# Performance work log

Hardware: AMD Instinct MI355X
Metric: run time of the kernel (lower is better)

## Reference

```python
import jax, jax.numpy as jnp
import numpy as np

ATOL = 1e-06
RTOL = 1e-06

def setup_inputs() -> dict:
    key = jax.random.key(0)
    ks = jax.random.split(key, 8)
    u = lambda k, shape: jax.random.uniform(k, shape, jnp.float32, -0.05, 0.05)
    return {
        "x": jax.random.normal(ks[0], (4096, 32, 32, 3), jnp.float32),
        "W_lstm": u(ks[1], (3, 16)),      # input kernel, gates [i,f,c,o]
        "U_lstm": u(ks[2], (4, 16)),      # recurrent kernel
        "dw_kernel": u(ks[3], (27, 27, 3, 5)),  # depthwise (kh,kw,in_c,mult)
        "pw_kernel": u(ks[4], (15, 4)),   # pointwise
        "conv_bias": u(ks[5], (4,)),
        "W_td": u(ks[6], (4096, 10)),
        "W_sc": u(ks[7], (4096, 10)),
    }

def _lstm_td(x, W, U):
    # TimeDistributed LSTM: x (B,32,32,3) -> treat axis1 as TD batch, axis2 as time
    B = x.shape[0]
    seq = x.reshape(B * 32, 32, 3)          # (N, T, F)
    xs = jnp.transpose(seq, (1, 0, 2))      # (T, N, F)
    N = seq.shape[0]
    h0 = jnp.zeros((N, 4), x.dtype)
    c0 = jnp.zeros((N, 4), x.dtype)

    def step(carry, xt):
        h, c = carry
        z = xt @ W + h @ U                  # (N, 16)
        zi, zf, zc, zo = jnp.split(z, 4, axis=-1)
        i = jax.nn.elu(zi)                  # recurrent_activation='elu'
        f = jax.nn.elu(zf)
        c = f * c + i * jax.nn.softmax(zc, axis=-1)  # activation='softmax'
        o = jax.nn.elu(zo)
        h = o * jax.nn.softmax(c, axis=-1)
        return (h, c), h

    _, hs = jax.lax.scan(step, (h0, c0), xs)        # (T, N, 4)
    return jnp.transpose(hs, (1, 0, 2)).reshape(B, 32, 32, 4)

def _sep_conv(x, dw_kernel, pw_kernel, conv_bias):
    # depthwise: Keras (kh,kw,C,M) -> lax HWIO grouped (kh,kw,1,C*M), channel-major order
    dw = dw_kernel.reshape(27, 27, 1, 15)
    y = jax.lax.conv_general_dilated(
        x, dw, window_strides=(1, 1), padding='SAME',
        feature_group_count=3,
        dimension_numbers=('NHWC', 'HWIO', 'NHWC'))   # (B,32,32,15)
    y = jnp.einsum('bhwc,cf->bhwf', y, pw_kernel) + conv_bias
    return jax.nn.sigmoid(y)                          # (B,32,32,4)

def reference(x, W_lstm, U_lstm, dw_kernel, pw_kernel, conv_bias, W_td, W_sc):
    B = x.shape[0]
    td = _lstm_td(x, W_lstm, U_lstm).reshape(B, -1) @ W_td   # (B,10)
    sc = _sep_conv(x, dw_kernel, pw_kernel, conv_bias).reshape(B, -1) @ W_sc
    diff = jnp.abs(td - sc)
    tol = ATOL + RTOL * jnp.abs(sc)
    return diff <= tol
```

## Files before the change

### kernel.cpp

```cpp
#include <hip/hip_runtime.h>
#include <math.h>

#define TD_OFF 0
#define WTDR_OFF 40960
#define BG_BYTE_OFF 524288

typedef __bf16 bf16x8 __attribute__((ext_vector_type(8)));
typedef float f32x16 __attribute__((ext_vector_type(16)));

union FragU { bf16x8 v; float4 f; };

__device__ __forceinline__ f32x16 mfma16(bf16x8 a, bf16x8 b, f32x16 c) {
    return __builtin_amdgcn_mfma_f32_32x32x16_bf16(a, b, c, 0, 0, 0);
}

__device__ __forceinline__ float eluf(float v) {
    return v > 0.f ? v : __expf(v) - 1.f;
}

__global__ __launch_bounds__(256) void prep(const float* __restrict__ dw,
                                            const float* __restrict__ pw,
                                            const float* __restrict__ Wtd,
                                            float* __restrict__ Wtdr,
                                            unsigned short* __restrict__ Bg) {
    int gid = blockIdx.x * 256 + threadIdx.x;
    if (gid < 40960) {
        int k = gid & 3;
        int r = gid >> 2;
        int row = r & 31; r >>= 5;
        int j = r % 10;
        int tt = r / 10;
        Wtdr[gid] = Wtd[(size_t)(row * 128 + tt * 4 + k) * 10 + j];
        return;
    }
    int g2 = gid - 40960;
    if (g2 >= 162 * 128) return;
    int n = g2 & 127;
    int s = g2 >> 7;
    int half = s & 1;
    int cd = s >> 1;
    int c = cd / 27, d = cd % 27;
    int w = n >> 2, f = n & 3;
    unsigned short* dsth = Bg + (size_t)s * 4096 + n * 16;
    unsigned short* dstl = dsth + 2048;
#pragma unroll
    for (int k = 0; k < 16; k++) {
        int xi = half * 16 + k;
        int dx = xi - w + 13;
        float v = 0.f;
        if (dx >= 0 && dx < 27) {
#pragma unroll
            for (int m = 0; m < 5; m++)
                v = fmaf(dw[((d * 27 + dx) * 3 + c) * 5 + m],
                         pw[(c * 5 + m) * 4 + f], v);
        }
        __bf16 h = (__bf16)v;
        __bf16 l = (__bf16)(v - (float)h);
        dsth[k] = __builtin_bit_cast(unsigned short, h);
        dstl[k] = __builtin_bit_cast(unsigned short, l);
    }
}

__global__ void lstm_td(const float* __restrict__ x,
                        const float* __restrict__ W,
                        const float* __restrict__ U,
                        const float* __restrict__ Wtdr,
                        float* __restrict__ td_out) {
    float rW[48], rU[64];
    const float4* W4 = (const float4*)W;
    const float4* U4 = (const float4*)U;
#pragma unroll
    for (int i = 0; i < 12; i++) {
        float4 q = W4[i];
        rW[i * 4 + 0] = q.x; rW[i * 4 + 1] = q.y;
        rW[i * 4 + 2] = q.z; rW[i * 4 + 3] = q.w;
    }
#pragma unroll
    for (int i = 0; i < 16; i++) {
        float4 q = U4[i];
        rU[i * 4 + 0] = q.x; rU[i * 4 + 1] = q.y;
        rU[i * 4 + 2] = q.z; rU[i * 4 + 3] = q.w;
    }

    int t = threadIdx.x;
    int n = blockIdx.x * 256 + t;
    int row = n & 31;
    const float4* xp4 = (const float4*)(x + (size_t)n * 96);

    float h0 = 0, h1 = 0, h2 = 0, h3 = 0;
    float c0 = 0, c1 = 0, c2 = 0, c3 = 0;
    float acc[10];
#pragma unroll
    for (int j = 0; j < 10; j++) acc[j] = 0.f;

    for (int g = 0; g < 8; g++) {
        float4 q0 = xp4[g * 3 + 0], q1 = xp4[g * 3 + 1], q2 = xp4[g * 3 + 2];
        float xr[12] = {q0.x, q0.y, q0.z, q0.w, q1.x, q1.y,
                        q1.z, q1.w, q2.x, q2.y, q2.z, q2.w};
#pragma unroll
        for (int st = 0; st < 4; st++) {
            int tt = g * 4 + st;
            float x0 = xr[st * 3 + 0], x1 = xr[st * 3 + 1], x2 = xr[st * 3 + 2];
            float z[16];
#pragma unroll
            for (int k = 0; k < 16; k++)
                z[k] = x0 * rW[k] + x1 * rW[16 + k] + x2 * rW[32 + k]
                     + h0 * rU[k] + h1 * rU[16 + k] + h2 * rU[32 + k] + h3 * rU[48 + k];

            float ig0 = eluf(z[0]),  ig1 = eluf(z[1]),  ig2 = eluf(z[2]),  ig3 = eluf(z[3]);
            float fg0 = eluf(z[4]),  fg1 = eluf(z[5]),  fg2 = eluf(z[6]),  fg3 = eluf(z[7]);
            float og0 = eluf(z[12]), og1 = eluf(z[13]), og2 = eluf(z[14]), og3 = eluf(z[15]);

            float zm = fmaxf(fmaxf(z[8], z[9]), fmaxf(z[10], z[11]));
            float e0 = __expf(z[8] - zm), e1 = __expf(z[9] - zm);
            float e2 = __expf(z[10] - zm), e3 = __expf(z[11] - zm);
            float inv = 1.f / (e0 + e1 + e2 + e3);
            c0 = fg0 * c0 + ig0 * (e0 * inv);
            c1 = fg1 * c1 + ig1 * (e1 * inv);
            c2 = fg2 * c2 + ig2 * (e2 * inv);
            c3 = fg3 * c3 + ig3 * (e3 * inv);

            float cm = fmaxf(fmaxf(c0, c1), fmaxf(c2, c3));
            float p0 = __expf(c0 - cm), p1 = __expf(c1 - cm);
            float p2 = __expf(c2 - cm), p3 = __expf(c3 - cm);
            float pinv = 1.f / (p0 + p1 + p2 + p3);
            h0 = og0 * (p0 * pinv); h1 = og1 * (p1 * pinv);
            h2 = og2 * (p2 * pinv); h3 = og3 * (p3 * pinv);

            const float4* wr4 = (const float4*)(Wtdr + (size_t)tt * 1280) + row;
#pragma unroll
            for (int j = 0; j < 10; j++) {
                float4 q = wr4[j * 32];
                acc[j] += h0 * q.x + h1 * q.y + h2 * q.z + h3 * q.w;
            }
        }
    }

#pragma unroll
    for (int off = 16; off >= 1; off >>= 1) {
#pragma unroll
        for (int j = 0; j < 10; j++) acc[j] += __shfl_xor(acc[j], off, 64);
    }
    int lane = t & 63;
    if (lane == 0 || lane == 32) {
        int b = n >> 5;
#pragma unroll
        for (int j = 0; j < 10; j++) td_out[b * 10 + j] = acc[j];
    }
}

#define A_OFF 0
#define ZOFF 49152
#define SRED_OFF 49168
#define LDS_BYTES 49488

__global__ __launch_bounds__(256, 3) void conv_sc(const float* __restrict__ x,
                                                  const unsigned short* __restrict__ Bg,
                                                  const float* __restrict__ Wsc,
                                                  const float* __restrict__ bias,
                                                  const float* __restrict__ td,
                                                  float* __restrict__ out) {
    __shared__ char LDS[LDS_BYTES] __attribute__((aligned(16)));
    int t = threadIdx.x;
    int l = t & 63;
    int wv = t >> 6;
    int m = l & 31;
    int sub = l >> 5;
    int img0 = (wv >> 1) * 2;
    int ntbase = (wv & 1) * 2;

    const char* bbase = (const char*)Bg + (size_t)ntbase * 1024 + m * 32 + sub * 16;
    FragU bufA[4], bufB[4];
#define LOADB(sv, arr) { const char* p_ = bbase + (size_t)(sv) * 8192;       \
        arr[0].f = *(const float4*)(p_);                         \
        arr[1].f = *(const float4*)(p_ + 4096);                  \
        arr[2].f = *(const float4*)(p_ + 1024);                  \
        arr[3].f = *(const float4*)(p_ + 5120); }

    LOADB(0, bufA);
    LOADB(1, bufB);

    const float4* xb4 = (const float4*)(x + (size_t)blockIdx.x * 12288);
#pragma unroll
    for (int it = 0; it < 12; it++) {
        int fi = it * 256 + t;
        float4 q = xb4[fi];
        float vals[4] = {q.x, q.y, q.z, q.w};
#pragma unroll
        for (int e = 0; e < 4; e++) {
            int pel = fi * 4 + e;
            int im = pel / 3072;
            int p = pel - im * 3072;
            int c = p % 3;
            int hw = p / 3;
            int w = hw & 31;
            int h = hw >> 5;
            int rec = A_OFF + im * 12288
                      + ((c * 8) + (w >> 4) * 2 + ((w >> 3) & 1)) * 512
                      + h * 16 + (w & 7) * 2;
            float v = vals[e];
            __bf16 hb = (__bf16)v;
            __bf16 lb = (__bf16)(v - (float)hb);
            *(__bf16*)(LDS + rec) = hb;
            *(__bf16*)(LDS + rec + 2048) = lb;
        }
    }
    if (t < 4) *(float*)(LDS + ZOFF + t * 4) = 0.f;
    __syncthreads();

    f32x16 acc00 = {0,0,0,0,0,0,0,0,0,0,0,0,0,0,0,0};
    f32x16 acc01 = acc00, acc10 = acc00, acc11 = acc00;

    int c = 0, d = 0, half = 0;

#define CHUNK(USE, SNEXT) {                                                   \
    int rowIdx = m + d - 13;                                                  \
    bool valid = (unsigned)rowIdx < 32u;                                      \
    int a0 = A_OFF + img0 * 12288 + (c * 8 + half * 2 + sub) * 512 + rowIdx * 16; \
    int ah0o = valid ? a0 : ZOFF;                                             \
    int al0o = valid ? (a0 + 2048) : ZOFF;                                    \
    int ah1o = valid ? (a0 + 12288) : ZOFF;                                   \
    int al1o = valid ? (a0 + 14336) : ZOFF;                                   \
    FragU ah0, al0, ah1, al1;                                                 \
    ah0.f = *(const float4*)(LDS + ah0o);                                     \
    al0.f = *(const float4*)(LDS + al0o);                                     \
    ah1.f = *(const float4*)(LDS + ah1o);                                     \
    al1.f = *(const float4*)(LDS + al1o);                                     \
    acc00 = mfma16(ah0.v, USE[0].v, acc00);                                   \
    acc01 = mfma16(ah0.v, USE[2].v, acc01);                                   \
    acc10 = mfma16(ah1.v, USE[0].v, acc10);                                   \
    acc11 = mfma16(ah1.v, USE[2].v, acc11);                                   \
    acc00 = mfma16(ah0.v, USE[1].v, acc00);                                   \
    acc01 = mfma16(ah0.v, USE[3].v, acc01);                                   \
    acc10 = mfma16(ah1.v, USE[1].v, acc10);                                   \
    acc11 = mfma16(ah1.v, USE[3].v, acc11);                                   \
    acc00 = mfma16(al0.v, USE[0].v, acc00);                                   \
    acc01 = mfma16(al0.v, USE[2].v, acc01);                                   \
    acc10 = mfma16(al1.v, USE[0].v, acc10);                                   \
    acc11 = mfma16(al1.v, USE[2].v, acc11);                                   \
    LOADB(SNEXT, USE);                                                        \
    half ^= 1;                                                                \
    if (!half) { d++; if (d == 27) { d = 0; c++; } }                          \
}

    for (int g = 0; g < 81; g++) {
        CHUNK(bufA, 2 * g + 2);
        CHUNK(bufB, 2 * g + 3);
    }

    float b4[4];
#pragma unroll
    for (int i = 0; i < 4; i++) b4[i] = bias[i];

    float part[2][10];
#pragma unroll
    for (int i = 0; i < 2; i++)
#pragma unroll
        for (int j = 0; j < 10; j++) part[i][j] = 0.f;

    f32x16 accs[2][2] = {{acc00, acc01}, {acc10, acc11}};
#pragma unroll
    for (int i2 = 0; i2 < 2; i2++) {
#pragma unroll
        for (int j2 = 0; j2 < 2; j2++) {
            int ncol = (ntbase + j2) * 32 + m;
            int wcol = ncol >> 2;
            int f = ncol & 3;
            f32x16 a = accs[i2][j2];
#pragma unroll
            for (int r = 0; r < 16; r++) {
                int h = (r & 3) + 8 * (r >> 2) + 4 * sub;
                float v = a[r] + b4[f];
                float sg = 1.f / (1.f + expf(-v));
                const float* wr = Wsc + (size_t)((h * 32 + wcol) * 4 + f) * 10;
#pragma unroll
                for (int j = 0; j < 10; j++) part[i2][j] = fmaf(sg, wr[j], part[i2][j]);
            }
        }
    }

#pragma unroll
    for (int off = 32; off >= 1; off >>= 1) {
#pragma unroll
        for (int i2 = 0; i2 < 2; i2++)
#pragma unroll
            for (int j = 0; j < 10; j++) part[i2][j] += __shfl_xor(part[i2][j], off, 64);
    }
    if (l == 0) {
        float* red = (float*)(LDS + SRED_OFF);
#pragma unroll
        for (int i2 = 0; i2 < 2; i2++)
#pragma unroll
            for (int j = 0; j < 10; j++) red[(wv * 2 + i2) * 10 + j] = part[i2][j];
    }
    __syncthreads();
    if (t < 40) {
        int img = t / 10, j = t % 10;
        const float* red = (const float*)(LDS + SRED_OFF);
        int pair = img >> 1, i2 = img & 1;
        float sv = red[((pair * 2) * 2 + i2) * 10 + j]
                 + red[((pair * 2 + 1) * 2 + i2) * 10 + j];
        int oi = (blockIdx.x * 4 + img) * 10 + j;
        float a = td[oi];
        float tol = 1e-6f + 1e-6f * fabsf(sv);
        out[oi] = (fabsf(a - sv) <= tol) ? 1.0f : 0.0f;
    }
}

extern "C" void kernel_launch(void* const* d_in, const int* in_sizes, int n_in,
                              void* d_out, int out_size, void* d_ws, size_t ws_size,
                              hipStream_t stream) {
    const float* x    = (const float*)d_in[0];
    const float* W    = (const float*)d_in[1];
    const float* U    = (const float*)d_in[2];
    const float* dw   = (const float*)d_in[3];
    const float* pw   = (const float*)d_in[4];
    const float* bias = (const float*)d_in[5];
    const float* Wtd  = (const float*)d_in[6];
    const float* Wsc  = (const float*)d_in[7];

    float* ws     = (float*)d_ws;
    float* td_acc = ws + TD_OFF;
    float* Wtdr   = ws + WTDR_OFF;
    unsigned short* Bg = (unsigned short*)((char*)d_ws + BG_BYTE_OFF);

    prep<<<241, 256, 0, stream>>>(dw, pw, Wtd, Wtdr, Bg);
    lstm_td<<<512, 256, 0, stream>>>(x, W, U, Wtdr, td_acc);
    conv_sc<<<1024, 256, 0, stream>>>(x, Bg, Wsc, bias, td_acc, (float*)d_out);
}
```

Measured before the change: 391.9 us.

## Fuse LSTM and conv kernels into one heterogeneous launch with separate compare

Merges the LSTM time-distributed kernel and the separable-conv MFMA kernel into a single launch, where every third block runs the LSTM path and the rest run the conv path. Both write partial results to workspace, and a small compare kernel produces the final output. The aim is to overlap the latency-bound, ALU-heavy LSTM work with the MFMA/LDS-bound conv work on the same CUs instead of running them back to back. In exchange, the fused kernel inherits the conv path's launch bounds and LDS allocation for the LSTM blocks, which may limit LSTM occupancy, and it adds an extra launch plus a workspace round trip.

New measurement: 369.3 us. -5.8%, faster.

```diff
diff --git a/kernel.cpp b/kernel.cpp
--- a/kernel.cpp
+++ b/kernel.cpp
@@ -3,6 +3,7 @@
 
 #define TD_OFF 0
 #define WTDR_OFF 40960
+#define SC_OFF 81920
 #define BG_BYTE_OFF 524288
 
 typedef __bf16 bf16x8 __attribute__((ext_vector_type(8)));
@@ -61,107 +62,111 @@
     }
 }
 
-__global__ void lstm_td(const float* __restrict__ x,
-                        const float* __restrict__ W,
-                        const float* __restrict__ U,
-                        const float* __restrict__ Wtdr,
-                        float* __restrict__ td_out) {
-    float rW[48], rU[64];
-    const float4* W4 = (const float4*)W;
-    const float4* U4 = (const float4*)U;
-#pragma unroll
-    for (int i = 0; i < 12; i++) {
-        float4 q = W4[i];
-        rW[i * 4 + 0] = q.x; rW[i * 4 + 1] = q.y;
-        rW[i * 4 + 2] = q.z; rW[i * 4 + 3] = q.w;
-    }
-#pragma unroll
-    for (int i = 0; i < 16; i++) {
-        float4 q = U4[i];
-        rU[i * 4 + 0] = q.x; rU[i * 4 + 1] = q.y;
-        rU[i * 4 + 2] = q.z; rU[i * 4 + 3] = q.w;
-    }
-
-    int t = threadIdx.x;
-    int n = blockIdx.x * 256 + t;
-    int row = n & 31;
-    const float4* xp4 = (const float4*)(x + (size_t)n * 96);
-
-    float h0 = 0, h1 = 0, h2 = 0, h3 = 0;
-    float c0 = 0, c1 = 0, c2 = 0, c3 = 0;
-    float acc[10];
-#pragma unroll
-    for (int j = 0; j < 10; j++) acc[j] = 0.f;
-
-    for (int g = 0; g < 8; g++) {
-        float4 q0 = xp4[g * 3 + 0], q1 = xp4[g * 3 + 1], q2 = xp4[g * 3 + 2];
-        float xr[12] = {q0.x, q0.y, q0.z, q0.w, q1.x, q1.y,
-                        q1.z, q1.w, q2.x, q2.y, q2.z, q2.w};
-#pragma unroll
-        for (int st = 0; st < 4; st++) {
-            int tt = g * 4 + st;
-            float x0 = xr[st * 3 + 0], x1 = xr[st * 3 + 1], x2 = xr[st * 3 + 2];
-            float z[16];
-#pragma unroll
-            for (int k = 0; k < 16; k++)
-                z[k] = x0 * rW[k] + x1 * rW[16 + k] + x2 * rW[32 + k]
-                     + h0 * rU[k] + h1 * rU[16 + k] + h2 * rU[32 + k] + h3 * rU[48 + k];
-
-            float ig0 = eluf(z[0]),  ig1 = eluf(z[1]),  ig2 = eluf(z[2]),  ig3 = eluf(z[3]);
-            float fg0 = eluf(z[4]),  fg1 = eluf(z[5]),  fg2 = eluf(z[6]),  fg3 = eluf(z[7]);
-            float og0 = eluf(z[12]), og1 = eluf(z[13]), og2 = eluf(z[14]), og3 = eluf(z[15]);
-
-            float zm = fmaxf(fmaxf(z[8], z[9]), fmaxf(z[10], z[11]));
-            float e0 = __expf(z[8] - zm), e1 = __expf(z[9] - zm);
-            float e2 = __expf(z[10] - zm), e3 = __expf(z[11] - zm);
-            float inv = 1.f / (e0 + e1 + e2 + e3);
-            c0 = fg0 * c0 + ig0 * (e0 * inv);
-            c1 = fg1 * c1 + ig1 * (e1 * inv);
-            c2 = fg2 * c2 + ig2 * (e2 * inv);
-            c3 = fg3 * c3 + ig3 * (e3 * inv);
-
-            float cm = fmaxf(fmaxf(c0, c1), fmaxf(c2, c3));
-            float p0 = __expf(c0 - cm), p1 = __expf(c1 - cm);
-            float p2 = __expf(c2 - cm), p3 = __expf(c3 - cm);
-            float pinv = 1.f / (p0 + p1 + p2 + p3);
-            h0 = og0 * (p0 * pinv); h1 = og1 * (p1 * pinv);
-            h2 = og2 * (p2 * pinv); h3 = og3 * (p3 * pinv);
-
-            const float4* wr4 = (const float4*)(Wtdr + (size_t)tt * 1280) + row;
-#pragma unroll
-            for (int j = 0; j < 10; j++) {
-                float4 q = wr4[j * 32];
-                acc[j] += h0 * q.x + h1 * q.y + h2 * q.z + h3 * q.w;
-            }
-        }
-    }
-
-#pragma unroll
-    for (int off = 16; off >= 1; off >>= 1) {
-#pragma unroll
-        for (int j = 0; j < 10; j++) acc[j] += __shfl_xor(acc[j], off, 64);
-    }
-    int lane = t & 63;
-    if (lane == 0 || lane == 32) {
-        int b = n >> 5;
-#pragma unroll
-        for (int j = 0; j < 10; j++) td_out[b * 10 + j] = acc[j];
-    }
-}
-
 #define A_OFF 0
 #define ZOFF 49152
 #define SRED_OFF 49168
 #define LDS_BYTES 49488
 
-__global__ __launch_bounds__(256, 3) void conv_sc(const float* __restrict__ x,
-                                                  const unsigned short* __restrict__ Bg,
-                                                  const float* __restrict__ Wsc,
-                                                  const float* __restrict__ bias,
-                                                  const float* __restrict__ td,
-                                                  float* __restrict__ out) {
+__global__ __launch_bounds__(256, 3) void fused(const float* __restrict__ x,
+                                                const float* __restrict__ W,
+                                                const float* __restrict__ U,
+                                                const float* __restrict__ Wtdr,
+                                                const unsigned short* __restrict__ Bg,
+                                                const float* __restrict__ Wsc,
+                                                const float* __restrict__ bias,
+                                                float* __restrict__ td_out,
+                                                float* __restrict__ sc_out) {
     __shared__ char LDS[LDS_BYTES] __attribute__((aligned(16)));
+    int bx = blockIdx.x;
+    int rem = bx % 3;
+    int q = bx / 3;
     int t = threadIdx.x;
+
+    if (rem == 2) {
+        float rW[48], rU[64];
+        const float4* W4 = (const float4*)W;
+        const float4* U4 = (const float4*)U;
+#pragma unroll
+        for (int i = 0; i < 12; i++) {
+            float4 qv = W4[i];
+            rW[i * 4 + 0] = qv.x; rW[i * 4 + 1] = qv.y;
+            rW[i * 4 + 2] = qv.z; rW[i * 4 + 3] = qv.w;
+        }
+#pragma unroll
+        for (int i = 0; i < 16; i++) {
+            float4 qv = U4[i];
+            rU[i * 4 + 0] = qv.x; rU[i * 4 + 1] = qv.y;
+            rU[i * 4 + 2] = qv.z; rU[i * 4 + 3] = qv.w;
+        }
+
+        int n = q * 256 + t;
+        int row = n & 31;
+        const float4* xp4 = (const float4*)(x + (size_t)n * 96);
+
+        float h0 = 0, h1 = 0, h2 = 0, h3 = 0;
+        float c0 = 0, c1 = 0, c2 = 0, c3 = 0;
+        float acc[10];
+#pragma unroll
+        for (int j = 0; j < 10; j++) acc[j] = 0.f;
+
+        for (int g = 0; g < 8; g++) {
+            float4 q0 = xp4[g * 3 + 0], q1 = xp4[g * 3 + 1], q2 = xp4[g * 3 + 2];
+            float xr[12] = {q0.x, q0.y, q0.z, q0.w, q1.x, q1.y,
+                            q1.z, q1.w, q2.x, q2.y, q2.z, q2.w};
+#pragma unroll
+            for (int st = 0; st < 4; st++) {
+                int tt = g * 4 + st;
+                float x0 = xr[st * 3 + 0], x1 = xr[st * 3 + 1], x2 = xr[st * 3 + 2];
+                float z[16];
+#pragma unroll
+                for (int k = 0; k < 16; k++)
+                    z[k] = x0 * rW[k] + x1 * rW[16 + k] + x2 * rW[32 + k]
+                         + h0 * rU[k] + h1 * rU[16 + k] + h2 * rU[32 + k] + h3 * rU[48 + k];
+
+                float ig0 = eluf(z[0]),  ig1 = eluf(z[1]),  ig2 = eluf(z[2]),  ig3 = eluf(z[3]);
+                float fg0 = eluf(z[4]),  fg1 = eluf(z[5]),  fg2 = eluf(z[6]),  fg3 = eluf(z[7]);
+                float og0 = eluf(z[12]), og1 = eluf(z[13]), og2 = eluf(z[14]), og3 = eluf(z[15]);
+
+                float zm = fmaxf(fmaxf(z[8], z[9]), fmaxf(z[10], z[11]));
+                float e0 = __expf(z[8] - zm), e1 = __expf(z[9] - zm);
+                float e2 = __expf(z[10] - zm), e3 = __expf(z[11] - zm);
+                float inv = 1.f / (e0 + e1 + e2 + e3);
+                c0 = fg0 * c0 + ig0 * (e0 * inv);
+                c1 = fg1 * c1 + ig1 * (e1 * inv);
+                c2 = fg2 * c2 + ig2 * (e2 * inv);
+                c3 = fg3 * c3 + ig3 * (e3 * inv);
+
+                float cm = fmaxf(fmaxf(c0, c1), fmaxf(c2, c3));
+                float p0 = __expf(c0 - cm), p1 = __expf(c1 - cm);
+                float p2 = __expf(c2 - cm), p3 = __expf(c3 - cm);
+                float pinv = 1.f / (p0 + p1 + p2 + p3);
+                h0 = og0 * (p0 * pinv); h1 = og1 * (p1 * pinv);
+                h2 = og2 * (p2 * pinv); h3 = og3 * (p3 * pinv);
+
+                const float4* wr4 = (const float4*)(Wtdr + (size_t)tt * 1280) + row;
+#pragma unroll
+                for (int j = 0; j < 10; j++) {
+                    float4 qv = wr4[j * 32];
+                    acc[j] += h0 * qv.x + h1 * qv.y + h2 * qv.z + h3 * qv.w;
+                }
+            }
+        }
+
+#pragma unroll
+        for (int off = 16; off >= 1; off >>= 1) {
+#pragma unroll
+            for (int j = 0; j < 10; j++) acc[j] += __shfl_xor(acc[j], off, 64);
+        }
+        int lane = t & 63;
+        if (lane == 0 || lane == 32) {
+            int b = n >> 5;
+#pragma unroll
+            for (int j = 0; j < 10; j++) td_out[b * 10 + j] = acc[j];
+        }
+        return;
+    }
+
+    int ci = q * 2 + rem;
     int l = t & 63;
     int wv = t >> 6;
     int m = l & 31;
@@ -180,12 +185,12 @@
     LOADB(0, bufA);
     LOADB(1, bufB);
 
-    const float4* xb4 = (const float4*)(x + (size_t)blockIdx.x * 12288);
+    const float4* xb4 = (const float4*)(x + (size_t)ci * 12288);
 #pragma unroll
     for (int it = 0; it < 12; it++) {
         int fi = it * 256 + t;
-        float4 q = xb4[fi];
-        float vals[4] = {q.x, q.y, q.z, q.w};
+        float4 qv = xb4[fi];
+        float vals[4] = {qv.x, qv.y, qv.z, qv.w};
 #pragma unroll
         for (int e = 0; e < 4; e++) {
             int pel = fi * 4 + e;
@@ -300,10 +305,19 @@
         int pair = img >> 1, i2 = img & 1;
         float sv = red[((pair * 2) * 2 + i2) * 10 + j]
                  + red[((pair * 2 + 1) * 2 + i2) * 10 + j];
-        int oi = (blockIdx.x * 4 + img) * 10 + j;
-        float a = td[oi];
-        float tol = 1e-6f + 1e-6f * fabsf(sv);
-        out[oi] = (fabsf(a - sv) <= tol) ? 1.0f : 0.0f;
+        sc_out[(ci * 4 + img) * 10 + j] = sv;
+    }
+}
+
+__global__ __launch_bounds__(256) void cmp_k(const float* __restrict__ td,
+                                             const float* __restrict__ sc,
+                                             float* __restrict__ out) {
+    int i = blockIdx.x * 256 + threadIdx.x;
+    if (i < 40960) {
+        float a = td[i];
+        float s = sc[i];
+        float tol = 1e-6f + 1e-6f * fabsf(s);
+        out[i] = (fabsf(a - s) <= tol) ? 1.0f : 0.0f;
     }
 }
 
@@ -322,9 +336,10 @@
     float* ws     = (float*)d_ws;
     float* td_acc = ws + TD_OFF;
     float* Wtdr   = ws + WTDR_OFF;
+    float* sc_acc = ws + SC_OFF;
     unsigned short* Bg = (unsigned short*)((char*)d_ws + BG_BYTE_OFF);
 
     prep<<<241, 256, 0, stream>>>(dw, pw, Wtd, Wtdr, Bg);
-    lstm_td<<<512, 256, 0, stream>>>(x, W, U, Wtdr, td_acc);
-    conv_sc<<<1024, 256, 0, stream>>>(x, Bg, Wsc, bias, td_acc, (float*)d_out);
-}
+    fused<<<1536, 256, 0, stream>>>(x, W, U, Wtdr, Bg, Wsc, bias, td_acc, sc_acc);
+    cmp_k<<<160, 256, 0, stream>>>(td_acc, sc_acc, (float*)d_out);
+}
```
